# Optimization experiments

Hardware: AMD Instinct MI355X
Metric: run time of the kernel (lower is better)

The kernel has to match this reference:

```python
import jax, jax.numpy as jnp
import numpy as np

V, E, H, C = 50000, 300, 512, 3
B, T_TEXT, T_TOPIC = 64, 256, 16


def setup_inputs() -> dict:
    key = jax.random.key(0)
    ks = jax.random.split(key, 12)
    s = lambda *sh: 1.0 / np.sqrt(sh[0])
    return {
        "text": jax.random.randint(ks[0], (B, T_TEXT), 0, V),
        "topic": jax.random.randint(ks[1], (B, T_TOPIC), 0, V),
        "emb": jax.random.normal(ks[2], (V, E), jnp.float32) * 0.1,
        "text_Wz": jax.random.normal(ks[3], (E + H, H), jnp.float32) * s(E + H),
        "text_bz": jnp.zeros((H,), jnp.float32),
        "text_Wo": jax.random.normal(ks[4], (E + H, H), jnp.float32) * s(E + H),
        "text_bo": jnp.zeros((H,), jnp.float32),
        "topic_Wz": jax.random.normal(ks[5], (E + H, H), jnp.float32) * s(E + H),
        "topic_bz": jnp.zeros((H,), jnp.float32),
        "topic_Wo": jax.random.normal(ks[6], (E + H, H), jnp.float32) * s(E + H),
        "topic_bo": jnp.zeros((H,), jnp.float32),
        "att_W": jax.random.normal(ks[7], (2 * H, 1), jnp.float32) * s(2 * H),
        "att_b": jnp.zeros((1,), jnp.float32),
        "fc1_W": jax.random.normal(ks[8], (2 * H, H), jnp.float32) * s(2 * H),
        "fc1_b": jnp.zeros((H,), jnp.float32),
        "fc2_W": jax.random.normal(ks[9], (H, C), jnp.float32) * s(H),
        "fc2_b": jnp.zeros((C,), jnp.float32),
    }


def _min_gru(emb_seq, Wz, bz, Wo, bo):
    # emb_seq: [B, T, E]; scan over time with hidden-dependent gates.
    b = emb_seq.shape[0]
    h0 = jnp.zeros((b, Wz.shape[1]), emb_seq.dtype)

    def step(h, x_t):
        comb = jnp.concatenate([x_t, h], axis=1)          # [B, E+H]
        z = jax.nn.sigmoid(comb @ Wz + bz)
        h_tilde = jnp.tanh(comb @ Wo + bo)
        h_new = (1.0 - z) * h + z * h_tilde
        return h_new, h_new

    xs = jnp.swapaxes(emb_seq, 0, 1)                      # [T, B, E]
    h_last, outs = jax.lax.scan(step, h0, xs)
    return jnp.swapaxes(outs, 0, 1), h_last               # [B, T, H], [B, H]


def reference(text, topic, emb, text_Wz, text_bz, text_Wo, text_bo,
              topic_Wz, topic_bz, topic_Wo, topic_bo,
              att_W, att_b, fc1_W, fc1_b, fc2_W, fc2_b):
    text_emb = emb[text]                                  # [B, Tt, E]
    topic_emb = emb[topic]                                # [B, Tp, E]
    text_out, _ = _min_gru(text_emb, text_Wz, text_bz, text_Wo, text_bo)
    _, topic_h = _min_gru(topic_emb, topic_Wz, topic_bz, topic_Wo, topic_bo)

    # topic attention over text timesteps
    t = text_out.shape[1]
    topic_exp = jnp.broadcast_to(topic_h[:, None, :], (topic_h.shape[0], t, topic_h.shape[1]))
    combined = jnp.concatenate([text_out, topic_exp], axis=2)   # [B, T, 2H]
    scores = combined @ att_W + att_b                            # [B, T, 1]
    weights = jax.nn.softmax(scores, axis=1)
    context = jnp.sum(weights * text_out, axis=1)                # [B, H]

    feat = jnp.concatenate([context, topic_h], axis=1)           # [B, 2H]
    # dropout is identity in eval mode
    hid = jax.nn.relu(feat @ fc1_W + fc1_b)
    logits = hid @ fc2_W + fc2_b
    return logits, weights
```

## Files before the change

kernel.cpp:

```cpp
#include <hip/hip_runtime.h>
#include <math.h>

#define NB 64
#define TTX 256
#define TTP 16
#define EE 300
#define HH 512
#define SENT16 0x7FC1u
#define SENT32 0x7FC17FC1u

typedef __attribute__((ext_vector_type(4))) float f32x4;
typedef __attribute__((ext_vector_type(8))) short short8;

__device__ __forceinline__ unsigned short bf16cvt(float f) {
  unsigned u = __float_as_uint(f);
  u += 0x7FFFu + ((u >> 16) & 1u);
  return (unsigned short)(u >> 16);
}

__global__ __launch_bounds__(256) void sd_prep(
    const float* __restrict__ tWz, const float* __restrict__ tWo,
    const float* __restrict__ pWz, const float* __restrict__ pWo,
    unsigned short* __restrict__ Bt, unsigned* __restrict__ ring32)
{
  const int i = blockIdx.x * 256 + threadIdx.x;
  if (i < 4 * NB * HH / 2) ring32[i] = SENT32;
  const int half = 327680;
  const int j = (i < half) ? i : i - half;
  const int e    = j & 7;
  const int lane = (j >> 3) & 63;
  const int kc   = (j >> 9) % 10;
  const int tile = (j >> 9) / 10;
  const int k = kc * 32 + 8 * (lane >> 4) + e;
  const int c = tile * 16 + (lane & 15);
  const float* W = (i < half) ? ((c < 512) ? tWz : tWo)
                              : ((c < 512) ? pWz : pWo);
  const float v = (k < 300) ? W[(size_t)k * HH + (c & 511)] : 0.f;
  Bt[i] = bf16cvt(v);
}

__global__ __launch_bounds__(256) void sd_xproj_mfma(
    const int* __restrict__ text_idx, const int* __restrict__ topic_idx,
    const float* __restrict__ emb,
    const unsigned short* __restrict__ bt_text, const unsigned short* __restrict__ bt_topic,
    const float* __restrict__ tbz, const float* __restrict__ tbo,
    const float* __restrict__ pbz, const float* __restrict__ pbo,
    float* __restrict__ xp_text, float* __restrict__ xp_topic)
{
  __shared__ alignas(16) unsigned short Als[64 * 328];
  __shared__ int tok[64];

  const bool is_text = blockIdx.x < TTX;
  const int t   = is_text ? blockIdx.x : blockIdx.x - TTX;
  const int T   = is_text ? TTX : TTP;
  const int* idx = is_text ? text_idx : topic_idx;
  const unsigned short* Bt = is_text ? bt_text : bt_topic;
  const float* bz = is_text ? tbz : pbz;
  const float* bo = is_text ? tbo : pbo;
  float* xp = is_text ? xp_text : xp_topic;

  const int tid = threadIdx.x;
  const int c0  = blockIdx.y * 256;

  if (tid < 64) tok[tid] = idx[tid * T + t];
  __syncthreads();

  {
    const int m  = tid >> 2;
    const int qt = tid & 3;
    const float* er = emb + (size_t)tok[m] * EE;
    unsigned short* ar = Als + m * 328;
    for (int j = qt; j < 75; j += 4) {
      const float4 v = *(const float4*)(er + 4 * j);
      ushort4 o;
      o.x = bf16cvt(v.x); o.y = bf16cvt(v.y);
      o.z = bf16cvt(v.z); o.w = bf16cvt(v.w);
      *(ushort4*)(ar + 4 * j) = o;
    }
    if (qt == 0) {
      for (int k = 300; k < 328; ++k) ar[k] = 0;
    }
  }
  __syncthreads();

  const int w  = tid >> 6;
  const int l  = tid & 63;
  const int lr = l & 15;
  const int lg = l >> 4;
  const int tile0 = blockIdx.y * 16 + w * 4;

  f32x4 acc[4][4];
#pragma unroll
  for (int ms = 0; ms < 4; ++ms)
#pragma unroll
    for (int ns = 0; ns < 4; ++ns)
      acc[ms][ns] = (f32x4){0.f, 0.f, 0.f, 0.f};

#pragma unroll 2
  for (int kc = 0; kc < 10; ++kc) {
    short8 bfr[4];
#pragma unroll
    for (int ns = 0; ns < 4; ++ns)
      bfr[ns] = *reinterpret_cast<const short8*>(
          Bt + (((size_t)(tile0 + ns) * 10 + kc) * 64 + l) * 8);
    short8 afr[4];
#pragma unroll
    for (int ms = 0; ms < 4; ++ms)
      afr[ms] = *reinterpret_cast<const short8*>(Als + (ms * 16 + lr) * 328 + kc * 32 + 8 * lg);
#pragma unroll
    for (int ms = 0; ms < 4; ++ms)
#pragma unroll
      for (int ns = 0; ns < 4; ++ns)
        acc[ms][ns] = __builtin_amdgcn_mfma_f32_16x16x32_bf16(afr[ms], bfr[ns], acc[ms][ns], 0, 0, 0);
  }

#pragma unroll
  for (int ns = 0; ns < 4; ++ns) {
    const int cg = c0 + w * 64 + ns * 16 + lr;
    const float bias = (cg < 512) ? bz[cg] : bo[cg - 512];
#pragma unroll
    for (int ms = 0; ms < 4; ++ms) {
#pragma unroll
      for (int r = 0; r < 4; ++r) {
        const int row = ms * 16 + lg * 4 + r;
        xp[((size_t)t * 64 + row) * 1024 + cg] = acc[ms][ns][r] + bias;
      }
    }
  }
}

__global__ __launch_bounds__(512) void sd_recur(
    const float* __restrict__ tWz, const float* __restrict__ tWo,
    const float* __restrict__ pWz, const float* __restrict__ pWo,
    const float* __restrict__ xp_text, const float* __restrict__ xp_topic,
    float* __restrict__ text_out, unsigned short* __restrict__ hring,
    float* __restrict__ topic_h)
{
  __shared__ alignas(16) unsigned short h_bf[2][2080];
  __shared__ alignas(16) float red[2][2048];

  const int tid = threadIdx.x;
  const int bid = blockIdx.x;
  const int x = bid & 7;
  const int q = bid >> 3;
  const int g = x + 8 * (q >> 4);
  const int slice = q & 15;
  const int b0 = g * 4;
  const int c_base = slice * 32;

  const int wv = tid >> 6;
  const int lane = tid & 63;
  const int lg = lane >> 4;
  const int l15 = lane & 15;

  const int bi_w = tid >> 5;
  const int dw = tid & 31;

  const size_t wslot_off = (size_t)(b0 + bi_w) * HH + c_base + dw;

  int u = 0;

  for (int ph = 0; ph < 2; ++ph) {
    const float* Wz = ph ? pWz : tWz;
    const float* Wo = ph ? pWo : tWo;
    const float* xp = ph ? xp_topic : xp_text;
    const int T = ph ? TTP : TTX;

    float hprev_r = 0.f;

    short8 wfrag[4][2];
#pragma unroll
    for (int ns = 0; ns < 4; ++ns) {
      const float* Wg = (ns < 2) ? Wz : Wo;
      const int dim = (ns & 1) * 16 + l15;
#pragma unroll
      for (int kc = 0; kc < 2; ++kc) {
        const int kb = wv * 64 + kc * 32 + 8 * lg;
        short8 f;
#pragma unroll
        for (int e = 0; e < 8; ++e)
          f[e] = (short)bf16cvt(Wg[(size_t)(EE + kb + e) * HH + c_base + dim]);
        wfrag[ns][kc] = f;
      }
    }

    for (int t = 0; t < T; ++t, ++u) {
      const int cur = u & 1;
      const bool do_poll = (u > 0);
      const bool use_h   = (t > 0);

      float xpz = 0.f, xpo = 0.f;
      if (tid < 128) {
        const float* xpr = xp + ((size_t)t * 64 + (b0 + bi_w)) * 1024 + c_base + dw;
        xpz = xpr[0];
        xpo = xpr[512];
      }

      if (do_poll) {
        const unsigned long long* src64 = (const unsigned long long*)
            (hring + (size_t)(u & 3) * NB * HH + (size_t)b0 * HH);
        unsigned long long v;
        for (;;) {
          v = __hip_atomic_load(src64 + tid, __ATOMIC_RELAXED, __HIP_MEMORY_SCOPE_AGENT);
          const unsigned lo = (unsigned)v, hi = (unsigned)(v >> 32);
          if ((lo & 0xFFFFu) != SENT16 && (lo >> 16) != SENT16 &&
              (hi & 0xFFFFu) != SENT16 && (hi >> 16) != SENT16) break;
          __builtin_amdgcn_s_sleep(1);
        }
        *(unsigned long long*)&h_bf[cur][(tid >> 7) * 520 + (tid & 127) * 4] = v;
      }

      __syncthreads();

      if (do_poll && tid < 128 && !(tid & 1))
        __hip_atomic_store((unsigned*)(hring + (size_t)((u - 1) & 3) * NB * HH + wslot_off),
                           SENT32, __ATOMIC_RELAXED, __HIP_MEMORY_SCOPE_AGENT);

      if (use_h) {
        const unsigned short* hb = &h_bf[cur][(lane & 3) * 520 + wv * 64 + 8 * lg];
        const short8 a0 = *reinterpret_cast<const short8*>(hb + 0);
        const short8 a1 = *reinterpret_cast<const short8*>(hb + 32);

        f32x4 acc[4];
#pragma unroll
        for (int ns = 0; ns < 4; ++ns) {
          acc[ns] = (f32x4){0.f, 0.f, 0.f, 0.f};
          acc[ns] = __builtin_amdgcn_mfma_f32_16x16x32_bf16(a0, wfrag[ns][0], acc[ns], 0, 0, 0);
          acc[ns] = __builtin_amdgcn_mfma_f32_16x16x32_bf16(a1, wfrag[ns][1], acc[ns], 0, 0, 0);
        }
        if (lane < 16) {
#pragma unroll
          for (int ns = 0; ns < 4; ++ns)
#pragma unroll
            for (int r = 0; r < 4; ++r)
              red[cur][wv * 256 + r * 64 + ns * 16 + lane] = acc[ns][r];
        }
      }

      __syncthreads();

      if (tid < 128) {
        float zp = 0.f, op = 0.f;
        if (use_h) {
#pragma unroll
          for (int k2 = 0; k2 < 8; ++k2) {
            zp += red[cur][k2 * 256 + bi_w * 64 + dw];
            op += red[cur][k2 * 256 + bi_w * 64 + 32 + dw];
          }
        }
        const float a = zp + xpz;
        const float z = 1.f / (1.f + __expf(-a));
        const float bv = op + xpo;
        const float ab = fabsf(bv);
        const float e2 = __expf(-2.f * ab);
        const float htl = __builtin_copysignf((1.f - e2) / (1.f + e2), bv);
        const float hn = (1.f - z) * hprev_r + z * htl;
        hprev_r = hn;

        const unsigned short hb16 = bf16cvt(hn);
        const unsigned packed = (unsigned)hb16 |
                                ((unsigned)__shfl_down((int)hb16, 1, 64) << 16);

        asm volatile("s_waitcnt vmcnt(1)" ::: "memory");
        if (!(tid & 1))
          __hip_atomic_store((unsigned*)(hring + (size_t)((u + 1) & 3) * NB * HH + wslot_off),
                             packed, __ATOMIC_RELAXED, __HIP_MEMORY_SCOPE_AGENT);
        if (ph == 0)
          text_out[((size_t)(b0 + bi_w) * TTX + t) * HH + c_base + dw] = hn;
        else if (t == T - 1)
          topic_h[(size_t)(b0 + bi_w) * HH + c_base + dw] = hn;
      }
    }
  }
}

__global__ __launch_bounds__(256) void sd_att_fc(
    const float* __restrict__ text_out, const float* __restrict__ topic_h,
    const float* __restrict__ att_W, const float* __restrict__ att_b,
    const float* __restrict__ fc1_W, const float* __restrict__ fc1_b,
    const float* __restrict__ fc2_W, const float* __restrict__ fc2_b,
    float* __restrict__ logits, float* __restrict__ weights_out)
{
  __shared__ alignas(16) float aw[1024];
  __shared__ alignas(16) float th[512];
  __shared__ float sc_s[256];
  __shared__ float sred[256];
  __shared__ float wsh[256];
  __shared__ alignas(16) float feat[1024];
  __shared__ float hid[512];
  const int b = blockIdx.x, tid = threadIdx.x;

  for (int i = tid; i < 1024; i += 256) aw[i] = att_W[i];
  for (int i = tid; i < 512; i += 256) th[i] = topic_h[(size_t)b * HH + i];
  __syncthreads();

  float part = 0.f;
  for (int i = tid; i < 512; i += 256) part += th[i] * aw[512 + i];
  sred[tid] = part;
  __syncthreads();
  for (int s = 128; s > 0; s >>= 1) { if (tid < s) sred[tid] += sred[tid + s]; __syncthreads(); }
  const float cb = sred[0] + att_b[0];
  __syncthreads();

  const int gr = tid >> 5, ln = tid & 31;
  for (int rep = 0; rep < 32; ++rep) {
    const int t = rep * 8 + gr;
    const float* row = text_out + ((size_t)b * TTX + t) * HH;
    float p = 0.f;
#pragma unroll
    for (int j = 0; j < 4; ++j) {
      const float4 v  = *(const float4*)(row + ln * 4 + 128 * j);
      const float4 w4 = *(const float4*)(aw  + ln * 4 + 128 * j);
      p += v.x * w4.x + v.y * w4.y + v.z * w4.z + v.w * w4.w;
    }
#pragma unroll
    for (int o = 16; o > 0; o >>= 1) p += __shfl_xor(p, o, 32);
    if (ln == 0) sc_s[t] = p + cb;
  }
  __syncthreads();

  const float sc = sc_s[tid];
  sred[tid] = sc; __syncthreads();
  for (int s = 128; s > 0; s >>= 1) { if (tid < s) sred[tid] = fmaxf(sred[tid], sred[tid + s]); __syncthreads(); }
  const float m = sred[0];
  __syncthreads();
  const float e = expf(sc - m);
  sred[tid] = e; __syncthreads();
  for (int s = 128; s > 0; s >>= 1) { if (tid < s) sred[tid] += sred[tid + s]; __syncthreads(); }
  const float wv = e / sred[0];
  wsh[tid] = wv;
  weights_out[(size_t)b * TTX + tid] = wv;
  __syncthreads();

  for (int rep = 0; rep < 2; ++rep) {
    const int dcol = rep * 256 + tid;
    float accc = 0.f;
    const float* base = text_out + (size_t)b * TTX * HH + dcol;
    for (int t2 = 0; t2 < TTX; ++t2) accc += wsh[t2] * base[(size_t)t2 * HH];
    feat[dcol] = accc;
  }
  for (int i = tid; i < 512; i += 256) feat[512 + i] = th[i];
  __syncthreads();

  for (int rep = 0; rep < 2; ++rep) {
    const int dcol = rep * 256 + tid;
    float a = fc1_b[dcol];
#pragma unroll 4
    for (int j = 0; j < 1024; ++j) a += feat[j] * fc1_W[(size_t)j * HH + dcol];
    hid[dcol] = fmaxf(a, 0.f);
  }
  __syncthreads();

  float p0 = 0.f, p1 = 0.f, p2 = 0.f;
  for (int dv = tid; dv < 512; dv += 256) {
    const float hv = hid[dv];
    p0 += hv * fc2_W[dv * 3 + 0];
    p1 += hv * fc2_W[dv * 3 + 1];
    p2 += hv * fc2_W[dv * 3 + 2];
  }
  feat[tid] = p0; feat[256 + tid] = p1; feat[512 + tid] = p2;
  __syncthreads();
  for (int s = 128; s > 0; s >>= 1) {
    if (tid < s) {
      feat[tid] += feat[tid + s];
      feat[256 + tid] += feat[256 + tid + s];
      feat[512 + tid] += feat[512 + tid + s];
    }
    __syncthreads();
  }
  if (tid < 3) logits[b * 3 + tid] = feat[tid * 256] + fc2_b[tid];
}

extern "C" void kernel_launch(void* const* d_in, const int* in_sizes, int n_in,
                              void* d_out, int out_size, void* d_ws, size_t ws_size,
                              hipStream_t stream) {
  const int*   text  = (const int*)d_in[0];
  const int*   topic = (const int*)d_in[1];
  const float* emb   = (const float*)d_in[2];
  const float* tWz   = (const float*)d_in[3];
  const float* tbz   = (const float*)d_in[4];
  const float* tWo   = (const float*)d_in[5];
  const float* tbo   = (const float*)d_in[6];
  const float* pWz   = (const float*)d_in[7];
  const float* pbz   = (const float*)d_in[8];
  const float* pWo   = (const float*)d_in[9];
  const float* pbo   = (const float*)d_in[10];
  const float* attW  = (const float*)d_in[11];
  const float* attb  = (const float*)d_in[12];
  const float* fc1W  = (const float*)d_in[13];
  const float* fc1b  = (const float*)d_in[14];
  const float* fc2W  = (const float*)d_in[15];
  const float* fc2b  = (const float*)d_in[16];

  float* out = (float*)d_out;
  float* ws  = (float*)d_ws;

  float* xp_text  = ws;
  float* xp_topic = xp_text + (size_t)TTX * 64 * 1024;
  float* text_o   = xp_topic + (size_t)TTP * 64 * 1024;
  float* topic_hv = text_o + (size_t)NB * TTX * HH;
  unsigned short* hring = (unsigned short*)(topic_hv + (size_t)NB * HH);

  unsigned short* bt_text  = (unsigned short*)text_o;
  unsigned short* bt_topic = bt_text + 327680;

  sd_prep<<<dim3(2560), dim3(256), 0, stream>>>(tWz, tWo, pWz, pWo,
                                                bt_text, (unsigned*)hring);
  sd_xproj_mfma<<<dim3(TTX + TTP, 4), dim3(256), 0, stream>>>(
      text, topic, emb, bt_text, bt_topic, tbz, tbo, pbz, pbo, xp_text, xp_topic);
  sd_recur<<<dim3(256), dim3(512), 0, stream>>>(tWz, tWo, pWz, pWo, xp_text, xp_topic,
                                                text_o, hring, topic_hv);
  sd_att_fc<<<dim3(64), dim3(256), 0, stream>>>(text_o, topic_hv, attW, attb,
                                                fc1W, fc1b, fc2W, fc2b, out, out + 192);
}
```

Measured before the change: 639.0 us.

## Run text and topic recurrences concurrently on separate block groups

The recurrent kernel previously processed the text sequence and then the topic sequence in the same persistent blocks. The grid is now doubled so the topic recurrence runs on its own 256 blocks with its own hidden-state ring, in parallel with the text recurrence. This removes the 16 serial topic steps from the critical path. The risk is that the persistent spin-wait design now needs all 512 blocks co-resident (launch bounds ask for 4 blocks/CU); otherwise it could deadlock or contend.

After: 639.5 us. Within noise of the previous version (+0.1%).

```diff
diff --git a/kernel.cpp b/kernel.cpp
--- a/kernel.cpp
+++ b/kernel.cpp
@@ -8,6 +8,7 @@
 #define HH 512
 #define SENT16 0x7FC1u
 #define SENT32 0x7FC17FC1u
+#define RINGW (4 * NB * HH)
 
 typedef __attribute__((ext_vector_type(4))) float f32x4;
 typedef __attribute__((ext_vector_type(8))) short short8;
@@ -24,7 +25,7 @@
     unsigned short* __restrict__ Bt, unsigned* __restrict__ ring32)
 {
   const int i = blockIdx.x * 256 + threadIdx.x;
-  if (i < 4 * NB * HH / 2) ring32[i] = SENT32;
+  if (i < RINGW) ring32[i] = SENT32;
   const int half = 327680;
   const int j = (i < half) ? i : i - half;
   const int e    = j & 7;
@@ -129,7 +130,7 @@
   }
 }
 
-__global__ __launch_bounds__(512) void sd_recur(
+__global__ __launch_bounds__(512, 4) void sd_recur(
     const float* __restrict__ tWz, const float* __restrict__ tWo,
     const float* __restrict__ pWz, const float* __restrict__ pWo,
     const float* __restrict__ xp_text, const float* __restrict__ xp_topic,
@@ -141,13 +142,21 @@
 
   const int tid = threadIdx.x;
   const int bid = blockIdx.x;
-  const int x = bid & 7;
-  const int q = bid >> 3;
+  const bool is_text = bid < 256;
+  const int lbid = is_text ? bid : bid - 256;
+  const int x = lbid & 7;
+  const int q = lbid >> 3;
   const int g = x + 8 * (q >> 4);
   const int slice = q & 15;
   const int b0 = g * 4;
   const int c_base = slice * 32;
 
+  const float* Wz = is_text ? tWz : pWz;
+  const float* Wo = is_text ? tWo : pWo;
+  const float* xp = is_text ? xp_text : xp_topic;
+  const int T = is_text ? TTX : TTP;
+  unsigned short* ring = hring + (is_text ? 0 : RINGW);
+
   const int wv = tid >> 6;
   const int lane = tid & 63;
   const int lg = lane >> 4;
@@ -158,118 +167,109 @@
 
   const size_t wslot_off = (size_t)(b0 + bi_w) * HH + c_base + dw;
 
-  int u = 0;
-
-  for (int ph = 0; ph < 2; ++ph) {
-    const float* Wz = ph ? pWz : tWz;
-    const float* Wo = ph ? pWo : tWo;
-    const float* xp = ph ? xp_topic : xp_text;
-    const int T = ph ? TTP : TTX;
-
-    float hprev_r = 0.f;
-
-    short8 wfrag[4][2];
-#pragma unroll
-    for (int ns = 0; ns < 4; ++ns) {
-      const float* Wg = (ns < 2) ? Wz : Wo;
-      const int dim = (ns & 1) * 16 + l15;
-#pragma unroll
-      for (int kc = 0; kc < 2; ++kc) {
-        const int kb = wv * 64 + kc * 32 + 8 * lg;
-        short8 f;
-#pragma unroll
-        for (int e = 0; e < 8; ++e)
-          f[e] = (short)bf16cvt(Wg[(size_t)(EE + kb + e) * HH + c_base + dim]);
-        wfrag[ns][kc] = f;
+  short8 wfrag[4][2];
+#pragma unroll
+  for (int ns = 0; ns < 4; ++ns) {
+    const float* Wg = (ns < 2) ? Wz : Wo;
+    const int dim = (ns & 1) * 16 + l15;
+#pragma unroll
+    for (int kc = 0; kc < 2; ++kc) {
+      const int kb = wv * 64 + kc * 32 + 8 * lg;
+      short8 f;
+#pragma unroll
+      for (int e = 0; e < 8; ++e)
+        f[e] = (short)bf16cvt(Wg[(size_t)(EE + kb + e) * HH + c_base + dim]);
+      wfrag[ns][kc] = f;
+    }
+  }
+
+  float hprev_r = 0.f;
+
+  for (int t = 0; t < T; ++t) {
+    const int u = t;
+    const int cur = u & 1;
+    const bool do_poll = (u > 0);
+
+    float xpz = 0.f, xpo = 0.f;
+    if (tid < 128) {
+      const float* xpr = xp + ((size_t)t * 64 + (b0 + bi_w)) * 1024 + c_base + dw;
+      xpz = xpr[0];
+      xpo = xpr[512];
+    }
+
+    if (do_poll) {
+      const unsigned long long* src64 = (const unsigned long long*)
+          (ring + (size_t)(u & 3) * NB * HH + (size_t)b0 * HH);
+      unsigned long long v;
+      for (;;) {
+        v = __hip_atomic_load(src64 + tid, __ATOMIC_RELAXED, __HIP_MEMORY_SCOPE_AGENT);
+        const unsigned lo = (unsigned)v, hi = (unsigned)(v >> 32);
+        if ((lo & 0xFFFFu) != SENT16 && (lo >> 16) != SENT16 &&
+            (hi & 0xFFFFu) != SENT16 && (hi >> 16) != SENT16) break;
+        __builtin_amdgcn_s_sleep(1);
       }
-    }
-
-    for (int t = 0; t < T; ++t, ++u) {
-      const int cur = u & 1;
-      const bool do_poll = (u > 0);
-      const bool use_h   = (t > 0);
-
-      float xpz = 0.f, xpo = 0.f;
-      if (tid < 128) {
-        const float* xpr = xp + ((size_t)t * 64 + (b0 + bi_w)) * 1024 + c_base + dw;
-        xpz = xpr[0];
-        xpo = xpr[512];
+      *(unsigned long long*)&h_bf[cur][(tid >> 7) * 520 + (tid & 127) * 4] = v;
+    }
+
+    __syncthreads();
+
+    if (do_poll && tid < 128 && !(tid & 1))
+      __hip_atomic_store((unsigned*)(ring + (size_t)((u - 1) & 3) * NB * HH + wslot_off),
+                         SENT32, __ATOMIC_RELAXED, __HIP_MEMORY_SCOPE_AGENT);
+
+    if (do_poll) {
+      const unsigned short* hb = &h_bf[cur][(lane & 3) * 520 + wv * 64 + 8 * lg];
+      const short8 a0 = *reinterpret_cast<const short8*>(hb + 0);
+      const short8 a1 = *reinterpret_cast<const short8*>(hb + 32);
+
+      f32x4 acc[4];
+#pragma unroll
+      for (int ns = 0; ns < 4; ++ns) {
+        acc[ns] = (f32x4){0.f, 0.f, 0.f, 0.f};
+        acc[ns] = __builtin_amdgcn_mfma_f32_16x16x32_bf16(a0, wfrag[ns][0], acc[ns], 0, 0, 0);
+        acc[ns] = __builtin_amdgcn_mfma_f32_16x16x32_bf16(a1, wfrag[ns][1], acc[ns], 0, 0, 0);
       }
-
+      if (lane < 16) {
+#pragma unroll
+        for (int ns = 0; ns < 4; ++ns)
+#pragma unroll
+          for (int r = 0; r < 4; ++r)
+            red[cur][wv * 256 + r * 64 + ns * 16 + lane] = acc[ns][r];
+      }
+    }
+
+    __syncthreads();
+
+    if (tid < 128) {
+      float zp = 0.f, op = 0.f;
       if (do_poll) {
-        const unsigned long long* src64 = (const unsigned long long*)
-            (hring + (size_t)(u & 3) * NB * HH + (size_t)b0 * HH);
-        unsigned long long v;
-        for (;;) {
-          v = __hip_atomic_load(src64 + tid, __ATOMIC_RELAXED, __HIP_MEMORY_SCOPE_AGENT);
-          const unsigned lo = (unsigned)v, hi = (unsigned)(v >> 32);
-          if ((lo & 0xFFFFu) != SENT16 && (lo >> 16) != SENT16 &&
-              (hi & 0xFFFFu) != SENT16 && (hi >> 16) != SENT16) break;
-          __builtin_amdgcn_s_sleep(1);
-        }
-        *(unsigned long long*)&h_bf[cur][(tid >> 7) * 520 + (tid & 127) * 4] = v;
-      }
-
-      __syncthreads();
-
-      if (do_poll && tid < 128 && !(tid & 1))
-        __hip_atomic_store((unsigned*)(hring + (size_t)((u - 1) & 3) * NB * HH + wslot_off),
-                           SENT32, __ATOMIC_RELAXED, __HIP_MEMORY_SCOPE_AGENT);
-
-      if (use_h) {
-        const unsigned short* hb = &h_bf[cur][(lane & 3) * 520 + wv * 64 + 8 * lg];
-        const short8 a0 = *reinterpret_cast<const short8*>(hb + 0);
-        const short8 a1 = *reinterpret_cast<const short8*>(hb + 32);
-
-        f32x4 acc[4];
-#pragma unroll
-        for (int ns = 0; ns < 4; ++ns) {
-          acc[ns] = (f32x4){0.f, 0.f, 0.f, 0.f};
-          acc[ns] = __builtin_amdgcn_mfma_f32_16x16x32_bf16(a0, wfrag[ns][0], acc[ns], 0, 0, 0);
-          acc[ns] = __builtin_amdgcn_mfma_f32_16x16x32_bf16(a1, wfrag[ns][1], acc[ns], 0, 0, 0);
-        }
-        if (lane < 16) {
-#pragma unroll
-          for (int ns = 0; ns < 4; ++ns)
-#pragma unroll
-            for (int r = 0; r < 4; ++r)
-              red[cur][wv * 256 + r * 64 + ns * 16 + lane] = acc[ns][r];
+#pragma unroll
+        for (int k2 = 0; k2 < 8; ++k2) {
+          zp += red[cur][k2 * 256 + bi_w * 64 + dw];
+          op += red[cur][k2 * 256 + bi_w * 64 + 32 + dw];
         }
       }
-
-      __syncthreads();
-
-      if (tid < 128) {
-        float zp = 0.f, op = 0.f;
-        if (use_h) {
-#pragma unroll
-          for (int k2 = 0; k2 < 8; ++k2) {
-            zp += red[cur][k2 * 256 + bi_w * 64 + dw];
-            op += red[cur][k2 * 256 + bi_w * 64 + 32 + dw];
-          }
-        }
-        const float a = zp + xpz;
-        const float z = 1.f / (1.f + __expf(-a));
-        const float bv = op + xpo;
-        const float ab = fabsf(bv);
-        const float e2 = __expf(-2.f * ab);
-        const float htl = __builtin_copysignf((1.f - e2) / (1.f + e2), bv);
-        const float hn = (1.f - z) * hprev_r + z * htl;
-        hprev_r = hn;
-
-        const unsigned short hb16 = bf16cvt(hn);
-        const unsigned packed = (unsigned)hb16 |
-                                ((unsigned)__shfl_down((int)hb16, 1, 64) << 16);
-
-        asm volatile("s_waitcnt vmcnt(1)" ::: "memory");
-        if (!(tid & 1))
-          __hip_atomic_store((unsigned*)(hring + (size_t)((u + 1) & 3) * NB * HH + wslot_off),
-                             packed, __ATOMIC_RELAXED, __HIP_MEMORY_SCOPE_AGENT);
-        if (ph == 0)
-          text_out[((size_t)(b0 + bi_w) * TTX + t) * HH + c_base + dw] = hn;
-        else if (t == T - 1)
-          topic_h[(size_t)(b0 + bi_w) * HH + c_base + dw] = hn;
-      }
+      const float a = zp + xpz;
+      const float z = 1.f / (1.f + __expf(-a));
+      const float bv = op + xpo;
+      const float ab = fabsf(bv);
+      const float e2 = __expf(-2.f * ab);
+      const float htl = __builtin_copysignf((1.f - e2) / (1.f + e2), bv);
+      const float hn = (1.f - z) * hprev_r + z * htl;
+      hprev_r = hn;
+
+      const unsigned short hb16 = bf16cvt(hn);
+      const unsigned packed = (unsigned)hb16 |
+                              ((unsigned)__shfl_down((int)hb16, 1, 64) << 16);
+
+      asm volatile("s_waitcnt vmcnt(1)" ::: "memory");
+      if (!(tid & 1))
+        __hip_atomic_store((unsigned*)(ring + (size_t)((u + 1) & 3) * NB * HH + wslot_off),
+                           packed, __ATOMIC_RELAXED, __HIP_MEMORY_SCOPE_AGENT);
+      if (is_text)
+        text_out[((size_t)(b0 + bi_w) * TTX + t) * HH + c_base + dw] = hn;
+      else if (t == T - 1)
+        topic_h[(size_t)(b0 + bi_w) * HH + c_base + dw] = hn;
     }
   }
 }
@@ -408,7 +408,7 @@
                                                 bt_text, (unsigned*)hring);
   sd_xproj_mfma<<<dim3(TTX + TTP, 4), dim3(256), 0, stream>>>(
       text, topic, emb, bt_text, bt_topic, tbz, tbo, pbz, pbo, xp_text, xp_topic);
-  sd_recur<<<dim3(256), dim3(512), 0, stream>>>(tWz, tWo, pWz, pWo, xp_text, xp_topic,
+  sd_recur<<<dim3(512), dim3(512), 0, stream>>>(tWz, tWo, pWz, pWo, xp_text, xp_topic,
                                                 text_o, hring, topic_hv);
   sd_att_fc<<<dim3(64), dim3(256), 0, stream>>>(text_o, topic_hv, attW, attb,
                                                 fc1W, fc1b, fc2W, fc2b, out, out + 192);
```

## Fuse input projection into recurrent kernel, computing x-projection per timestep

Applied to the files above, without the earlier changes.

Removes the separate input-projection GEMM kernel and its large fp32 workspace. Inside the recurrent kernel, each step now gathers the token embeddings into shared memory as bf16 and computes the x-projection with MFMA against pre-swizzled weight fragments. The goal is to skip writing and re-reading the big xp buffer and one kernel launch, and to hide the extra work behind the cross-block synchronization wait. In exchange, each recurrent step does more work on its critical path: an embedding gather from global memory and 5 extra MFMAs per wave.

Result: slower. 811.8 us (+27.0%).

```diff
diff --git a/kernel.cpp b/kernel.cpp
--- a/kernel.cpp
+++ b/kernel.cpp
@@ -21,123 +21,43 @@
 __global__ __launch_bounds__(256) void sd_prep(
     const float* __restrict__ tWz, const float* __restrict__ tWo,
     const float* __restrict__ pWz, const float* __restrict__ pWo,
-    unsigned short* __restrict__ Bt, unsigned* __restrict__ ring32)
+    unsigned short* __restrict__ wxf, unsigned* __restrict__ ring32)
 {
   const int i = blockIdx.x * 256 + threadIdx.x;
-  if (i < 4 * NB * HH / 2) ring32[i] = SENT32;
-  const int half = 327680;
-  const int j = (i < half) ? i : i - half;
-  const int e    = j & 7;
-  const int lane = (j >> 3) & 63;
-  const int kc   = (j >> 9) % 10;
-  const int tile = (j >> 9) / 10;
+  if (i < 65536) ring32[i] = SENT32;
+  const int ph = i / 327680;
+  const int r  = i - ph * 327680;
+  const int slice = r / 20480;
+  const int r2 = r - slice * 20480;
+  const int ns = r2 / 5120;
+  const int r3 = r2 - ns * 5120;
+  const int kc = r3 / 512;
+  const int r4 = r3 - kc * 512;
+  const int lane = r4 >> 3;
+  const int e    = r4 & 7;
   const int k = kc * 32 + 8 * (lane >> 4) + e;
-  const int c = tile * 16 + (lane & 15);
-  const float* W = (i < half) ? ((c < 512) ? tWz : tWo)
-                              : ((c < 512) ? pWz : pWo);
-  const float v = (k < 300) ? W[(size_t)k * HH + (c & 511)] : 0.f;
-  Bt[i] = bf16cvt(v);
-}
-
-__global__ __launch_bounds__(256) void sd_xproj_mfma(
+  const int col = slice * 32 + (ns & 1) * 16 + (lane & 15);
+  const float* W = ph ? ((ns >> 1) ? pWo : pWz) : ((ns >> 1) ? tWo : tWz);
+  const float v = (k < 300) ? W[(size_t)k * HH + col] : 0.f;
+  wxf[i] = bf16cvt(v);
+}
+
+__global__ __launch_bounds__(512) void sd_recur(
     const int* __restrict__ text_idx, const int* __restrict__ topic_idx,
     const float* __restrict__ emb,
-    const unsigned short* __restrict__ bt_text, const unsigned short* __restrict__ bt_topic,
+    const float* __restrict__ tWz, const float* __restrict__ tWo,
+    const float* __restrict__ pWz, const float* __restrict__ pWo,
     const float* __restrict__ tbz, const float* __restrict__ tbo,
     const float* __restrict__ pbz, const float* __restrict__ pbo,
-    float* __restrict__ xp_text, float* __restrict__ xp_topic)
-{
-  __shared__ alignas(16) unsigned short Als[64 * 328];
-  __shared__ int tok[64];
-
-  const bool is_text = blockIdx.x < TTX;
-  const int t   = is_text ? blockIdx.x : blockIdx.x - TTX;
-  const int T   = is_text ? TTX : TTP;
-  const int* idx = is_text ? text_idx : topic_idx;
-  const unsigned short* Bt = is_text ? bt_text : bt_topic;
-  const float* bz = is_text ? tbz : pbz;
-  const float* bo = is_text ? tbo : pbo;
-  float* xp = is_text ? xp_text : xp_topic;
-
-  const int tid = threadIdx.x;
-  const int c0  = blockIdx.y * 256;
-
-  if (tid < 64) tok[tid] = idx[tid * T + t];
-  __syncthreads();
-
-  {
-    const int m  = tid >> 2;
-    const int qt = tid & 3;
-    const float* er = emb + (size_t)tok[m] * EE;
-    unsigned short* ar = Als + m * 328;
-    for (int j = qt; j < 75; j += 4) {
-      const float4 v = *(const float4*)(er + 4 * j);
-      ushort4 o;
-      o.x = bf16cvt(v.x); o.y = bf16cvt(v.y);
-      o.z = bf16cvt(v.z); o.w = bf16cvt(v.w);
-      *(ushort4*)(ar + 4 * j) = o;
-    }
-    if (qt == 0) {
-      for (int k = 300; k < 328; ++k) ar[k] = 0;
-    }
-  }
-  __syncthreads();
-
-  const int w  = tid >> 6;
-  const int l  = tid & 63;
-  const int lr = l & 15;
-  const int lg = l >> 4;
-  const int tile0 = blockIdx.y * 16 + w * 4;
-
-  f32x4 acc[4][4];
-#pragma unroll
-  for (int ms = 0; ms < 4; ++ms)
-#pragma unroll
-    for (int ns = 0; ns < 4; ++ns)
-      acc[ms][ns] = (f32x4){0.f, 0.f, 0.f, 0.f};
-
-#pragma unroll 2
-  for (int kc = 0; kc < 10; ++kc) {
-    short8 bfr[4];
-#pragma unroll
-    for (int ns = 0; ns < 4; ++ns)
-      bfr[ns] = *reinterpret_cast<const short8*>(
-          Bt + (((size_t)(tile0 + ns) * 10 + kc) * 64 + l) * 8);
-    short8 afr[4];
-#pragma unroll
-    for (int ms = 0; ms < 4; ++ms)
-      afr[ms] = *reinterpret_cast<const short8*>(Als + (ms * 16 + lr) * 328 + kc * 32 + 8 * lg);
-#pragma unroll
-    for (int ms = 0; ms < 4; ++ms)
-#pragma unroll
-      for (int ns = 0; ns < 4; ++ns)
-        acc[ms][ns] = __builtin_amdgcn_mfma_f32_16x16x32_bf16(afr[ms], bfr[ns], acc[ms][ns], 0, 0, 0);
-  }
-
-#pragma unroll
-  for (int ns = 0; ns < 4; ++ns) {
-    const int cg = c0 + w * 64 + ns * 16 + lr;
-    const float bias = (cg < 512) ? bz[cg] : bo[cg - 512];
-#pragma unroll
-    for (int ms = 0; ms < 4; ++ms) {
-#pragma unroll
-      for (int r = 0; r < 4; ++r) {
-        const int row = ms * 16 + lg * 4 + r;
-        xp[((size_t)t * 64 + row) * 1024 + cg] = acc[ms][ns][r] + bias;
-      }
-    }
-  }
-}
-
-__global__ __launch_bounds__(512) void sd_recur(
-    const float* __restrict__ tWz, const float* __restrict__ tWo,
-    const float* __restrict__ pWz, const float* __restrict__ pWo,
-    const float* __restrict__ xp_text, const float* __restrict__ xp_topic,
+    const unsigned short* __restrict__ wxf,
     float* __restrict__ text_out, unsigned short* __restrict__ hring,
     float* __restrict__ topic_h)
 {
   __shared__ alignas(16) unsigned short h_bf[2][2080];
   __shared__ alignas(16) float red[2][2048];
+  __shared__ alignas(16) float red2[2][512];
+  __shared__ alignas(16) unsigned short emb_bf[2][1280];
+  __shared__ int tok_lds[1088];
 
   const int tid = threadIdx.x;
   const int bid = blockIdx.x;
@@ -158,13 +78,30 @@
 
   const size_t wslot_off = (size_t)(b0 + bi_w) * HH + c_base + dw;
 
+  for (int i = tid; i < 4 * TTX; i += 512) {
+    const int row = i >> 8, t0 = i & 255;
+    tok_lds[row * 272 + t0] = text_idx[(b0 + row) * TTX + t0];
+  }
+  if (tid < 64) {
+    const int row = tid >> 4, t0 = tid & 15;
+    tok_lds[row * 272 + 256 + t0] = topic_idx[(b0 + row) * TTP + t0];
+  }
+  __syncthreads();
+
   int u = 0;
 
   for (int ph = 0; ph < 2; ++ph) {
     const float* Wz = ph ? pWz : tWz;
     const float* Wo = ph ? pWo : tWo;
-    const float* xp = ph ? xp_topic : xp_text;
     const int T = ph ? TTP : TTX;
+    const int tb = ph ? 256 : 0;
+    const unsigned short* wxp = wxf + ph * 327680 + slice * 20480;
+
+    float bzr = 0.f, bor = 0.f;
+    if (tid < 128) {
+      bzr = (ph ? pbz : tbz)[c_base + dw];
+      bor = (ph ? pbo : tbo)[c_base + dw];
+    }
 
     float hprev_r = 0.f;
 
@@ -189,11 +126,13 @@
       const bool do_poll = (u > 0);
       const bool use_h   = (t > 0);
 
-      float xpz = 0.f, xpo = 0.f;
-      if (tid < 128) {
-        const float* xpr = xp + ((size_t)t * 64 + (b0 + bi_w)) * 1024 + c_base + dw;
-        xpz = xpr[0];
-        xpo = xpr[512];
+      for (int i = tid; i < 1280; i += 512) {
+        const int row = i / 320;
+        const int k = i - row * 320;
+        const int tk = tok_lds[row * 272 + tb + t];
+        float v = 0.f;
+        if (k < 300) v = emb[(size_t)tk * EE + k];
+        emb_bf[cur][row * 320 + k] = bf16cvt(v);
       }
 
       if (do_poll) {
@@ -237,6 +176,25 @@
         }
       }
 
+      {
+        const int ns = wv & 3;
+        const int kh = wv >> 2;
+        const unsigned short* wxb = wxp + ns * 5120 + (kh * 5) * 512 + lane * 8;
+        const unsigned short* ea  = &emb_bf[cur][(lane & 3) * 320 + (kh * 5) * 32 + 8 * lg];
+        f32x4 accx = (f32x4){0.f, 0.f, 0.f, 0.f};
+#pragma unroll
+        for (int k5 = 0; k5 < 5; ++k5) {
+          const short8 ax = *reinterpret_cast<const short8*>(ea + k5 * 32);
+          const short8 bx = *reinterpret_cast<const short8*>(wxb + k5 * 512);
+          accx = __builtin_amdgcn_mfma_f32_16x16x32_bf16(ax, bx, accx, 0, 0, 0);
+        }
+        if (lane < 16) {
+#pragma unroll
+          for (int r = 0; r < 4; ++r)
+            red2[cur][wv * 64 + r * 16 + lane] = accx[r];
+        }
+      }
+
       __syncthreads();
 
       if (tid < 128) {
@@ -248,6 +206,11 @@
             op += red[cur][k2 * 256 + bi_w * 64 + 32 + dw];
           }
         }
+        const int nsz = dw >> 4;
+        const int cl = bi_w * 16 + (dw & 15);
+        const float xpz = red2[cur][nsz * 64 + cl] + red2[cur][(4 + nsz) * 64 + cl] + bzr;
+        const float xpo = red2[cur][(2 + nsz) * 64 + cl] + red2[cur][(6 + nsz) * 64 + cl] + bor;
+
         const float a = zp + xpz;
         const float z = 1.f / (1.f + __expf(-a));
         const float bv = op + xpo;
@@ -395,21 +358,16 @@
   float* out = (float*)d_out;
   float* ws  = (float*)d_ws;
 
-  float* xp_text  = ws;
-  float* xp_topic = xp_text + (size_t)TTX * 64 * 1024;
-  float* text_o   = xp_topic + (size_t)TTP * 64 * 1024;
+  float* text_o   = ws;
   float* topic_hv = text_o + (size_t)NB * TTX * HH;
   unsigned short* hring = (unsigned short*)(topic_hv + (size_t)NB * HH);
-
-  unsigned short* bt_text  = (unsigned short*)text_o;
-  unsigned short* bt_topic = bt_text + 327680;
+  unsigned short* wxf   = hring + 131072;
 
   sd_prep<<<dim3(2560), dim3(256), 0, stream>>>(tWz, tWo, pWz, pWo,
-                                                bt_text, (unsigned*)hring);
-  sd_xproj_mfma<<<dim3(TTX + TTP, 4), dim3(256), 0, stream>>>(
-      text, topic, emb, bt_text, bt_topic, tbz, tbo, pbz, pbo, xp_text, xp_topic);
-  sd_recur<<<dim3(256), dim3(512), 0, stream>>>(tWz, tWo, pWz, pWo, xp_text, xp_topic,
-                                                text_o, hring, topic_hv);
+                                                wxf, (unsigned*)hring);
+  sd_recur<<<dim3(256), dim3(512), 0, stream>>>(
+      text, topic, emb, tWz, tWo, pWz, pWo, tbz, tbo, pbz, pbo,
+      wxf, text_o, hring, topic_hv);
   sd_att_fc<<<dim3(64), dim3(256), 0, stream>>>(text_o, topic_hv, attW, attb,
                                                 fc1W, fc1b, fc2W, fc2b, out, out + 192);
 }
```
